# Kernel tuning notes

Measured on AMD Instinct MI355X. Metric: run time of the kernel, lower is better.

## Reference

```python
import jax, jax.numpy as jnp
import numpy as np

BN_EPS = 1e-5


def setup_inputs() -> dict:
    key = jax.random.key(0)
    ks = jax.random.split(key, 16)
    B, C, H, W = 8, 256, 56, 56
    Ci = C // 2  # inter_channels = 128
    s = lambda fan_in: 1.0 / np.sqrt(fan_in)
    return {
        "x": jax.random.normal(ks[0], (B, C, H, W), jnp.float32),
        # 1x1 convs stored as [out, in] matrices
        "g_w": jax.random.normal(ks[1], (Ci, C), jnp.float32) * s(C),
        "g_b": jax.random.normal(ks[2], (Ci,), jnp.float32) * s(C),
        "theta_w": jax.random.normal(ks[3], (Ci, C), jnp.float32) * s(C),
        "theta_b": jax.random.normal(ks[4], (Ci,), jnp.float32) * s(C),
        "phi_w": jax.random.normal(ks[5], (Ci, C), jnp.float32) * s(C),
        "phi_b": jax.random.normal(ks[6], (Ci,), jnp.float32) * s(C),
        # W_f: Conv2d(2*Ci -> 1, k=1)
        "wf_w": jax.random.normal(ks[7], (1, 2 * Ci), jnp.float32) * s(2 * Ci),
        "wf_b": jax.random.normal(ks[8], (1,), jnp.float32) * s(2 * Ci),
        # W_z conv (Ci -> C); source zero-inits; random here for a non-trivial baseline
        "wz_w": jax.random.normal(ks[9], (C, Ci), jnp.float32) * s(Ci),
        "wz_b": jax.random.normal(ks[10], (C,), jnp.float32) * s(Ci),
        # BatchNorm2d (eval mode) params/stats; source zero-inits gamma/beta, randomized here
        "bn_gamma": jax.random.normal(ks[11], (C,), jnp.float32) * 0.1 + 1.0,
        "bn_beta": jax.random.normal(ks[12], (C,), jnp.float32) * 0.1,
        "bn_mean": jax.random.normal(ks[13], (C,), jnp.float32) * 0.1,
        "bn_var": jax.random.uniform(ks[14], (C,), jnp.float32, 0.5, 1.5),
    }


def reference(x, g_w, g_b, theta_w, theta_b, phi_w, phi_b,
              wf_w, wf_b, wz_w, wz_b, bn_gamma, bn_beta, bn_mean, bn_var):
    B, C, H, W = x.shape
    N = H * W
    Ci = g_w.shape[0]
    xf = x.reshape(B, C, N)  # [B, C, N]

    # 1x1 convs over flattened spatial dim
    g_x = jnp.einsum('oc,bcn->bno', g_w, xf) + g_b            # [B, N, Ci]
    theta = jnp.einsum('oc,bcn->bon', theta_w, xf) + theta_b[:, None]  # [B, Ci, N]
    phi = jnp.einsum('oc,bcn->bon', phi_w, xf) + phi_b[:, None]        # [B, Ci, N]

    # W_f over the (repeat+concat) tensor decomposes exactly:
    # f[b,i,j] = relu( w_t . theta[b,:,i] + w_p . phi[b,:,j] + b_f )
    w_t, w_p = wf_w[0, :Ci], wf_w[0, Ci:]
    a = jnp.einsum('c,bcn->bn', w_t, theta)   # [B, N]
    bsc = jnp.einsum('c,bcn->bn', w_p, phi)   # [B, N]
    f = jax.nn.relu(a[:, :, None] + bsc[:, None, :] + wf_b[0])  # [B, N, N]

    y = jnp.matmul(f / N, g_x)                # [B, N, Ci]
    y = y.transpose(0, 2, 1)                  # [B, Ci, N]

    W_y = jnp.einsum('oc,bcn->bon', wz_w, y) + wz_b[:, None]   # [B, C, N]
    inv = bn_gamma / jnp.sqrt(bn_var + BN_EPS)
    W_y = (W_y - bn_mean[:, None]) * inv[:, None] + bn_beta[:, None]

    z = W_y + xf
    return z.reshape(B, C, H, W)
```

## Files before the change

kernel.cpp:

```cpp
#include <hip/hip_runtime.h>
#include <cfloat>
#include <math.h>

#define BATCH 8
#define CH 256
#define CI 128
#define NPIX 3136
#define NCHUNK 98
#define NB 4096
#define BN_EPS 1e-5f

typedef __attribute__((ext_vector_type(8))) short bf16x8;
typedef __attribute__((ext_vector_type(4))) float f32x4;

__device__ __forceinline__ float bf2f(unsigned short u) {
    union { unsigned int i; float f; } x; x.i = ((unsigned int)u) << 16; return x.f;
}
__device__ __forceinline__ unsigned short f2bf(float f) {
    union { float f; unsigned int i; } x; x.f = f;
    unsigned int u = x.i;
    return (unsigned short)((u + 0x7FFFu + ((u >> 16) & 1u)) >> 16);
}

__global__ __launch_bounds__(256) void k_fold(
    const float* __restrict__ wf_w,
    const float* __restrict__ theta_w, const float* __restrict__ theta_b,
    const float* __restrict__ phi_w,   const float* __restrict__ phi_b,
    const float* __restrict__ g_w,     const float* __restrict__ wz_w,
    float* __restrict__ ta_w, float* __restrict__ pb_w, float* __restrict__ biases,
    unsigned short* __restrict__ Bfrag_g, unsigned short* __restrict__ Bfrag_w)
{
    const int bk = blockIdx.x, tid = threadIdx.x;
    if (bk == 0) {
        float ta = 0.f, pb = 0.f;
        for (int c = 0; c < CI; ++c) {
            ta += wf_w[c]      * theta_w[c * CH + tid];
            pb += wf_w[CI + c] * phi_w[c * CH + tid];
        }
        ta_w[tid] = ta;
        pb_w[tid] = pb;
        if (tid == 0) {
            float tb = 0.f, pbb = 0.f;
            for (int c = 0; c < CI; ++c) {
                tb  += wf_w[c]      * theta_b[c];
                pbb += wf_w[CI + c] * phi_b[c];
            }
            biases[0] = tb;
            biases[1] = pbb;
        }
    } else if (bk <= 8) {
        const int base_pair = (bk - 1) * 8;
        for (int e = tid; e < 4096; e += 256) {
            int pp = e >> 9, lane = (e >> 3) & 63, j = e & 7;
            int pair = base_pair + pp;
            int ks = pair >> 3, nt = pair & 7;
            int k = ks * 32 + (lane >> 4) * 8 + j;
            int n = nt * 16 + (lane & 15);
            Bfrag_g[(size_t)pair * 512 + lane * 8 + j] = f2bf(g_w[n * CH + k]);
        }
    } else {
        const int base_pair = (bk - 9) * 8;
        for (int e = tid; e < 4096; e += 256) {
            int pp = e >> 9, lane = (e >> 3) & 63, j = e & 7;
            int pair = base_pair + pp;
            int ks = pair >> 4, nt = pair & 15;
            int k = ks * 32 + (lane >> 4) * 8 + j;
            int n = nt * 16 + (lane & 15);
            Bfrag_w[(size_t)pair * 512 + lane * 8 + j] = f2bf(wz_w[n * CI + k]);
        }
    }
}

__global__ __launch_bounds__(256) void k_gemm(
    const float* __restrict__ x,
    const unsigned short* __restrict__ Bfrag_g,
    const float* __restrict__ g_b,
    const float* __restrict__ ta_w, const float* __restrict__ pb_w,
    const float* __restrict__ biases,
    unsigned short* __restrict__ gxg,
    float* __restrict__ a_out, float* __restrict__ bsc_out)
{
    __shared__ float xs[CH][36];
    __shared__ unsigned short xsb[32 * 264];
    __shared__ float ra[8][32], rp[8][32];
    unsigned short* gout = (unsigned short*)&xs[0][0];

    const int b  = blockIdx.y;
    const int n0 = blockIdx.x * 32;
    const int tid = threadIdx.x;

    for (int t = tid; t < CH * 8; t += 256) {
        int c = t >> 3, n4 = t & 7;
        const float4* src = (const float4*)(x + ((size_t)b * CH + c) * NPIX + n0);
        *((float4*)&xs[c][n4 * 4]) = src[n4];
    }
    __syncthreads();

    const int p = tid & 31;
    const int g = tid >> 5;

    {
        float aa = 0.f, pp = 0.f;
#pragma unroll 8
        for (int cc = 0; cc < 32; ++cc) {
            int c = g * 32 + cc;
            float v = xs[c][p];
            aa += ta_w[c] * v;
            pp += pb_w[c] * v;
        }
        ra[g][p] = aa; rp[g][p] = pp;
    }
    {
        const int cbase = g * 32;
        unsigned int* dst = (unsigned int*)&xsb[p * 264 + cbase];
#pragma unroll
        for (int q = 0; q < 16; ++q) {
            float lo = xs[cbase + 2 * q][p];
            float hi = xs[cbase + 2 * q + 1][p];
            dst[q] = (unsigned int)f2bf(lo) | ((unsigned int)f2bf(hi) << 16);
        }
    }
    __syncthreads();

    if (tid < 32) {
        float sa = 0.f, sp = 0.f;
#pragma unroll
        for (int gg = 0; gg < 8; ++gg) { sa += ra[gg][tid]; sp += rp[gg][tid]; }
        a_out[b * NPIX + n0 + tid]   = sa + biases[0];
        bsc_out[b * NPIX + n0 + tid] = sp + biases[1];
    }

    const int w = tid >> 6, l = tid & 63, lm = l & 15, lq = l >> 4;
    f32x4 acc[2][2];
#pragma unroll
    for (int mi = 0; mi < 2; ++mi)
#pragma unroll
        for (int ni = 0; ni < 2; ++ni) acc[mi][ni] = (f32x4){0.f, 0.f, 0.f, 0.f};

#pragma unroll
    for (int ks = 0; ks < 8; ++ks) {
        bf16x8 a0 = *(const bf16x8*)&xsb[lm * 264 + ks * 32 + lq * 8];
        bf16x8 a1 = *(const bf16x8*)&xsb[(16 + lm) * 264 + ks * 32 + lq * 8];
        bf16x8 b0 = *(const bf16x8*)(Bfrag_g + ((size_t)(ks * 8 + w * 2) * 64 + l) * 8);
        bf16x8 b1 = *(const bf16x8*)(Bfrag_g + ((size_t)(ks * 8 + w * 2 + 1) * 64 + l) * 8);
        acc[0][0] = __builtin_amdgcn_mfma_f32_16x16x32_bf16(a0, b0, acc[0][0], 0, 0, 0);
        acc[0][1] = __builtin_amdgcn_mfma_f32_16x16x32_bf16(a0, b1, acc[0][1], 0, 0, 0);
        acc[1][0] = __builtin_amdgcn_mfma_f32_16x16x32_bf16(a1, b0, acc[1][0], 0, 0, 0);
        acc[1][1] = __builtin_amdgcn_mfma_f32_16x16x32_bf16(a1, b1, acc[1][1], 0, 0, 0);
    }
    __syncthreads();

#pragma unroll
    for (int mi = 0; mi < 2; ++mi)
#pragma unroll
        for (int ni = 0; ni < 2; ++ni) {
            int o = w * 32 + ni * 16 + lm;
            float gb = g_b[o];
#pragma unroll
            for (int r = 0; r < 4; ++r) {
                int m = mi * 16 + lq * 4 + r;
                gout[m * 136 + o] = f2bf(acc[mi][ni][r] + gb);
            }
        }
    __syncthreads();

    {
        const int n = tid >> 3, ch = tid & 7;
        const uint4* s = (const uint4*)&gout[n * 136 + ch * 16];
        uint4* d = (uint4*)(gxg + ((size_t)(b * NPIX + n0 + n)) * CI + ch * 16);
        d[0] = s[0]; d[1] = s[1];
    }
}

__global__ __launch_bounds__(1024) void k_bucketsort(
    const float* __restrict__ bsc,
    float* __restrict__ s_sorted, int* __restrict__ idx_sorted,
    int* __restrict__ bstart, float* __restrict__ params)
{
    __shared__ float vals[NPIX];
    __shared__ unsigned short qarr[NPIX];
    __shared__ int hist[NB];
    __shared__ int cnt[NB];
    __shared__ float red[1024];
    __shared__ float red2[1024];
    __shared__ float sh_min, sh_scale;

    const int b = blockIdx.x, tid = threadIdx.x;

    float lmin = FLT_MAX, lmax = -FLT_MAX;
    for (int i = tid; i < NPIX; i += 1024) {
        float v = bsc[b * NPIX + i];
        vals[i] = v;
        lmin = fminf(lmin, v);
        lmax = fmaxf(lmax, v);
    }
    red[tid] = lmin; red2[tid] = lmax;
    __syncthreads();
    for (int off = 512; off > 0; off >>= 1) {
        if (tid < off) {
            red[tid]  = fminf(red[tid],  red[tid + off]);
            red2[tid] = fmaxf(red2[tid], red2[tid + off]);
        }
        __syncthreads();
    }
    if (tid == 0) {
        float mn = red[0], mx = red2[0];
        float range = mx - mn;
        float scale = (range > 0.f) ? (float)NB / range : 0.f;
        sh_min = mn; sh_scale = scale;
        params[b * 2] = mn; params[b * 2 + 1] = scale;
    }
    for (int i = tid; i < NB; i += 1024) { hist[i] = 0; cnt[i] = 0; }
    __syncthreads();

    const float bmin = sh_min, scale = sh_scale;
    for (int i = tid; i < NPIX; i += 1024) {
        int q = (int)((vals[i] - bmin) * scale);
        q = (q < 0) ? 0 : ((q > NB - 1) ? NB - 1 : q);
        qarr[i] = (unsigned short)q;
        atomicAdd(&hist[q], 1);
    }
    __syncthreads();

    int* psum = (int*)red;
    const int base4 = tid * 4;
    int h0 = hist[base4], h1 = hist[base4 + 1], h2 = hist[base4 + 2], h3 = hist[base4 + 3];
    psum[tid] = h0 + h1 + h2 + h3;
    __syncthreads();
    for (int off = 1; off < 1024; off <<= 1) {
        int v = psum[tid];
        int w = (tid >= off) ? psum[tid - off] : 0;
        __syncthreads();
        psum[tid] = v + w;
        __syncthreads();
    }
    int excl = (tid == 0) ? 0 : psum[tid - 1];
    hist[base4]     = excl;
    hist[base4 + 1] = excl + h0;
    hist[base4 + 2] = excl + h0 + h1;
    hist[base4 + 3] = excl + h0 + h1 + h2;
    __syncthreads();

    for (int i = tid; i < NB; i += 1024) bstart[b * (NB + 1) + i] = hist[i];
    if (tid == 0) bstart[b * (NB + 1) + NB] = NPIX;

    for (int i = tid; i < NPIX; i += 1024) {
        int q = qarr[i];
        int pos = hist[q] + atomicAdd(&cnt[q], 1);
        s_sorted[b * NPIX + pos]   = vals[i];
        idx_sorted[b * NPIX + pos] = i;
    }
}

__global__ __launch_bounds__(128) void k_csum(
    const unsigned short* __restrict__ gxg,
    const float* __restrict__ s_sorted, const int* __restrict__ idx_sorted,
    float* __restrict__ CS1, float* __restrict__ CS2)
{
    __shared__ int   sidx[32];
    __shared__ float sval[32];
    const int b = blockIdx.y, c = blockIdx.x, o = threadIdx.x;
    const int base = b * NPIX + c * 32;
    if (o < 32) {
        sidx[o] = idx_sorted[base + o];
        sval[o] = s_sorted[base + o];
    }
    __syncthreads();

    float a1 = 0.f, a2 = 0.f;
#pragma unroll 8
    for (int rr = 0; rr < 32; ++rr) {
        float v = bf2f(gxg[((size_t)(b * NPIX + sidx[rr])) * CI + o]);
        a1 += v;
        a2 += sval[rr] * v;
    }
    CS1[(b * 100 + c) * CI + o] = a1;
    CS2[(b * 100 + c) * CI + o] = a2;
}

__global__ __launch_bounds__(128) void k_suffix(
    float* __restrict__ CS1, float* __restrict__ CS2)
{
    __shared__ float buf[NCHUNK * CI];
    const int b = blockIdx.x, tid = threadIdx.x;
    float* __restrict__ CS = blockIdx.y ? CS2 : CS1;

    for (int i = tid; i < NCHUNK * CI; i += 128) buf[i] = CS[b * 100 * CI + i];
    __syncthreads();
    {
        float acc = 0.f;
        for (int c = NCHUNK - 1; c >= 0; --c) {
            acc += buf[c * CI + tid];
            buf[c * CI + tid] = acc;
        }
    }
    __syncthreads();
    for (int i = tid; i < NCHUNK * CI; i += 128) CS[b * 100 * CI + i] = buf[i];
    CS[(b * 100 + 98) * CI + tid] = 0.f;
    CS[(b * 100 + 99) * CI + tid] = 0.f;
}

__global__ __launch_bounds__(256) void k_final(
    const float* __restrict__ x,
    const float* __restrict__ a_arr, const float* __restrict__ wf_b,
    const float* __restrict__ CS1, const float* __restrict__ CS2,
    const int* __restrict__ bstart, const float* __restrict__ params,
    const unsigned short* __restrict__ Bfrag_w,
    const float* __restrict__ wz_b,
    const float* __restrict__ bn_g, const float* __restrict__ bn_b,
    const float* __restrict__ bn_m, const float* __restrict__ bn_v,
    float* __restrict__ out)
{
    __shared__ unsigned short ys[32 * 136];
    __shared__ float Df[32 * 260];
    __shared__ int   rs[32];
    __shared__ float ts[32];

    const int b = blockIdx.y;
    const int n0 = blockIdx.x * 32;
    const int tid = threadIdx.x;

    if (tid < 32) {
        float t = a_arr[b * NPIX + n0 + tid] + wf_b[0];
        float bmin = params[b * 2], scale = params[b * 2 + 1];
        float fq = (-t - bmin) * scale;
        int kb = (int)(fq + 0.5f);
        kb = (kb < 0) ? 0 : ((kb > NB) ? NB : kb);
        int r = bstart[b * (NB + 1) + kb];
        int cstar = (r + 16) >> 5;
        cstar = (cstar > 98) ? 98 : cstar;
        rs[tid] = cstar;
        ts[tid] = t;
    }
    __syncthreads();

    const int o = tid & 127;
    const int h = tid >> 7;
    const float invN = 1.0f / (float)NPIX;

#pragma unroll 4
    for (int i = 0; i < 16; ++i) {
        int n = h * 16 + i;
        int cb = (b * 100 + rs[n]) * CI + o;
        float S1 = CS1[cb], S2 = CS2[cb];
        ys[n * 136 + o] = f2bf((ts[n] * S1 + S2) * invN);
    }
    __syncthreads();

    const int w = tid >> 6, l = tid & 63, lm = l & 15, lq = l >> 4;
    f32x4 acc[2][4];
#pragma unroll
    for (int mi = 0; mi < 2; ++mi)
#pragma unroll
        for (int ni = 0; ni < 4; ++ni) acc[mi][ni] = (f32x4){0.f, 0.f, 0.f, 0.f};

#pragma unroll
    for (int ks = 0; ks < 4; ++ks) {
        bf16x8 a0 = *(const bf16x8*)&ys[lm * 136 + ks * 32 + lq * 8];
        bf16x8 a1 = *(const bf16x8*)&ys[(16 + lm) * 136 + ks * 32 + lq * 8];
#pragma unroll
        for (int ni = 0; ni < 4; ++ni) {
            bf16x8 bb = *(const bf16x8*)(Bfrag_w + ((size_t)(ks * 16 + w * 4 + ni) * 64 + l) * 8);
            acc[0][ni] = __builtin_amdgcn_mfma_f32_16x16x32_bf16(a0, bb, acc[0][ni], 0, 0, 0);
            acc[1][ni] = __builtin_amdgcn_mfma_f32_16x16x32_bf16(a1, bb, acc[1][ni], 0, 0, 0);
        }
    }

#pragma unroll
    for (int mi = 0; mi < 2; ++mi)
#pragma unroll
        for (int ni = 0; ni < 4; ++ni) {
            int cc = w * 64 + ni * 16 + lm;
#pragma unroll
            for (int r = 0; r < 4; ++r) {
                int m = mi * 16 + lq * 4 + r;
                Df[m * 260 + cc] = acc[mi][ni][r];
            }
        }
    __syncthreads();

    const int cc = tid;
    const float inv  = bn_g[cc] * rsqrtf(bn_v[cc] + BN_EPS);
    const float bias = (wz_b[cc] - bn_m[cc]) * inv + bn_b[cc];

    const float4* xp = (const float4*)(x   + ((size_t)b * CH + cc) * NPIX + n0);
    float4*       op = (float4*)      (out + ((size_t)b * CH + cc) * NPIX + n0);
#pragma unroll
    for (int n4 = 0; n4 < 8; ++n4) {
        float4 xv = xp[n4];
        float4 ov;
        ov.x = Df[(n4 * 4 + 0) * 260 + cc] * inv + bias + xv.x;
        ov.y = Df[(n4 * 4 + 1) * 260 + cc] * inv + bias + xv.y;
        ov.z = Df[(n4 * 4 + 2) * 260 + cc] * inv + bias + xv.z;
        ov.w = Df[(n4 * 4 + 3) * 260 + cc] * inv + bias + xv.w;
        op[n4] = ov;
    }
}

extern "C" void kernel_launch(void* const* d_in, const int* in_sizes, int n_in,
                              void* d_out, int out_size, void* d_ws, size_t ws_size,
                              hipStream_t stream)
{
    const float* x       = (const float*)d_in[0];
    const float* g_w     = (const float*)d_in[1];
    const float* g_b     = (const float*)d_in[2];
    const float* theta_w = (const float*)d_in[3];
    const float* theta_b = (const float*)d_in[4];
    const float* phi_w   = (const float*)d_in[5];
    const float* phi_b   = (const float*)d_in[6];
    const float* wf_w    = (const float*)d_in[7];
    const float* wf_b    = (const float*)d_in[8];
    const float* wz_w    = (const float*)d_in[9];
    const float* wz_b    = (const float*)d_in[10];
    const float* bn_g    = (const float*)d_in[11];
    const float* bn_b    = (const float*)d_in[12];
    const float* bn_m    = (const float*)d_in[13];
    const float* bn_v    = (const float*)d_in[14];

    float* ws = (float*)d_ws;
    float* ta_w   = ws;
    float* pb_w   = ws + 256;
    float* biases = ws + 512;
    float* params = ws + 516;
    float* a_arr  = ws + 532;
    float* bsc      = a_arr + BATCH * NPIX;
    float* s_sorted = bsc + BATCH * NPIX;
    int*   idx_sorted = (int*)(s_sorted + BATCH * NPIX);
    int*   bstart   = idx_sorted + BATCH * NPIX;
    float* CS1    = (float*)(bstart + BATCH * (NB + 1));
    float* CS2    = CS1 + BATCH * 100 * CI;
    unsigned short* Bfrag_g = (unsigned short*)(CS2 + BATCH * 100 * CI);
    unsigned short* Bfrag_w = Bfrag_g + 32768;
    unsigned short* gxg = Bfrag_w + 32768;

    k_fold<<<17, 256, 0, stream>>>(wf_w, theta_w, theta_b, phi_w, phi_b,
                                   g_w, wz_w, ta_w, pb_w, biases,
                                   Bfrag_g, Bfrag_w);

    k_gemm<<<dim3(NCHUNK, BATCH), 256, 0, stream>>>(
        x, Bfrag_g, g_b, ta_w, pb_w, biases, gxg, a_arr, bsc);

    k_bucketsort<<<BATCH, 1024, 0, stream>>>(bsc, s_sorted, idx_sorted,
                                             bstart, params);

    k_csum<<<dim3(NCHUNK, BATCH), 128, 0, stream>>>(
        gxg, s_sorted, idx_sorted, CS1, CS2);

    k_suffix<<<dim3(BATCH, 2), 128, 0, stream>>>(CS1, CS2);

    k_final<<<dim3(NCHUNK, BATCH), 256, 0, stream>>>(
        x, a_arr, wf_b, CS1, CS2, bstart, params, Bfrag_w,
        wz_b, bn_g, bn_b, bn_m, bn_v, (float*)d_out);
}
```

Before: 160.9 us.

## Use wave-shuffle reductions and scans, parallelize suffix sum, fuse epilogues

```diff
diff --git a/kernel.cpp b/kernel.cpp
--- a/kernel.cpp
+++ b/kernel.cpp
@@ -100,25 +100,19 @@
     const int g = tid >> 5;
 
     {
+        const int cbase = g * 32;
         float aa = 0.f, pp = 0.f;
-#pragma unroll 8
-        for (int cc = 0; cc < 32; ++cc) {
-            int c = g * 32 + cc;
-            float v = xs[c][p];
-            aa += ta_w[c] * v;
-            pp += pb_w[c] * v;
+        unsigned int* dst = (unsigned int*)&xsb[p * 264 + cbase];
+#pragma unroll
+        for (int q = 0; q < 16; ++q) {
+            int c0 = cbase + 2 * q;
+            float lo = xs[c0][p];
+            float hi = xs[c0 + 1][p];
+            aa += ta_w[c0] * lo + ta_w[c0 + 1] * hi;
+            pp += pb_w[c0] * lo + pb_w[c0 + 1] * hi;
+            dst[q] = (unsigned int)f2bf(lo) | ((unsigned int)f2bf(hi) << 16);
         }
         ra[g][p] = aa; rp[g][p] = pp;
-    }
-    {
-        const int cbase = g * 32;
-        unsigned int* dst = (unsigned int*)&xsb[p * 264 + cbase];
-#pragma unroll
-        for (int q = 0; q < 16; ++q) {
-            float lo = xs[cbase + 2 * q][p];
-            float hi = xs[cbase + 2 * q + 1][p];
-            dst[q] = (unsigned int)f2bf(lo) | ((unsigned int)f2bf(hi) << 16);
-        }
     }
     __syncthreads();
 
@@ -148,7 +142,6 @@
         acc[1][0] = __builtin_amdgcn_mfma_f32_16x16x32_bf16(a1, b0, acc[1][0], 0, 0, 0);
         acc[1][1] = __builtin_amdgcn_mfma_f32_16x16x32_bf16(a1, b1, acc[1][1], 0, 0, 0);
     }
-    __syncthreads();
 
 #pragma unroll
     for (int mi = 0; mi < 2; ++mi)
@@ -177,78 +170,112 @@
     float* __restrict__ s_sorted, int* __restrict__ idx_sorted,
     int* __restrict__ bstart, float* __restrict__ params)
 {
-    __shared__ float vals[NPIX];
-    __shared__ unsigned short qarr[NPIX];
     __shared__ int hist[NB];
     __shared__ int cnt[NB];
-    __shared__ float red[1024];
-    __shared__ float red2[1024];
+    __shared__ float wmin[16], wmax[16];
+    __shared__ int wtot[16], woff[16];
     __shared__ float sh_min, sh_scale;
 
     const int b = blockIdx.x, tid = threadIdx.x;
-
+    const int lane = tid & 63, wid = tid >> 6;
+
+#pragma unroll
+    for (int k = 0; k < 4; ++k) { hist[tid + k * 1024] = 0; cnt[tid + k * 1024] = 0; }
+
+    float v[4];
     float lmin = FLT_MAX, lmax = -FLT_MAX;
-    for (int i = tid; i < NPIX; i += 1024) {
-        float v = bsc[b * NPIX + i];
-        vals[i] = v;
-        lmin = fminf(lmin, v);
-        lmax = fmaxf(lmax, v);
-    }
-    red[tid] = lmin; red2[tid] = lmax;
-    __syncthreads();
-    for (int off = 512; off > 0; off >>= 1) {
-        if (tid < off) {
-            red[tid]  = fminf(red[tid],  red[tid + off]);
-            red2[tid] = fmaxf(red2[tid], red2[tid + off]);
-        }
-        __syncthreads();
-    }
-    if (tid == 0) {
-        float mn = red[0], mx = red2[0];
-        float range = mx - mn;
-        float scale = (range > 0.f) ? (float)NB / range : 0.f;
-        sh_min = mn; sh_scale = scale;
-        params[b * 2] = mn; params[b * 2 + 1] = scale;
-    }
-    for (int i = tid; i < NB; i += 1024) { hist[i] = 0; cnt[i] = 0; }
+#pragma unroll
+    for (int k = 0; k < 4; ++k) {
+        int i = tid + k * 1024;
+        if (i < NPIX) {
+            float t = bsc[b * NPIX + i];
+            v[k] = t;
+            lmin = fminf(lmin, t);
+            lmax = fmaxf(lmax, t);
+        }
+    }
+#pragma unroll
+    for (int m = 32; m >= 1; m >>= 1) {
+        lmin = fminf(lmin, __shfl_xor(lmin, m));
+        lmax = fmaxf(lmax, __shfl_xor(lmax, m));
+    }
+    if (lane == 0) { wmin[wid] = lmin; wmax[wid] = lmax; }
+    __syncthreads();
+
+    if (tid < 16) {
+        float a = wmin[tid], c = wmax[tid];
+#pragma unroll
+        for (int m = 8; m >= 1; m >>= 1) {
+            a = fminf(a, __shfl_xor(a, m));
+            c = fmaxf(c, __shfl_xor(c, m));
+        }
+        if (tid == 0) {
+            float range = c - a;
+            float scale = (range > 0.f) ? (float)NB / range : 0.f;
+            sh_min = a; sh_scale = scale;
+            params[b * 2] = a; params[b * 2 + 1] = scale;
+        }
+    }
     __syncthreads();
 
     const float bmin = sh_min, scale = sh_scale;
-    for (int i = tid; i < NPIX; i += 1024) {
-        int q = (int)((vals[i] - bmin) * scale);
-        q = (q < 0) ? 0 : ((q > NB - 1) ? NB - 1 : q);
-        qarr[i] = (unsigned short)q;
-        atomicAdd(&hist[q], 1);
-    }
-    __syncthreads();
-
-    int* psum = (int*)red;
+    int q[4];
+#pragma unroll
+    for (int k = 0; k < 4; ++k) {
+        int i = tid + k * 1024;
+        if (i < NPIX) {
+            int qq = (int)((v[k] - bmin) * scale);
+            qq = (qq < 0) ? 0 : ((qq > NB - 1) ? NB - 1 : qq);
+            q[k] = qq;
+            atomicAdd(&hist[qq], 1);
+        }
+    }
+    __syncthreads();
+
     const int base4 = tid * 4;
     int h0 = hist[base4], h1 = hist[base4 + 1], h2 = hist[base4 + 2], h3 = hist[base4 + 3];
-    psum[tid] = h0 + h1 + h2 + h3;
-    __syncthreads();
-    for (int off = 1; off < 1024; off <<= 1) {
-        int v = psum[tid];
-        int w = (tid >= off) ? psum[tid - off] : 0;
-        __syncthreads();
-        psum[tid] = v + w;
-        __syncthreads();
-    }
-    int excl = (tid == 0) ? 0 : psum[tid - 1];
+    int s = h0 + h1 + h2 + h3;
+    int incl = s;
+#pragma unroll
+    for (int off = 1; off < 64; off <<= 1) {
+        int t = __shfl_up(incl, off);
+        if (lane >= off) incl += t;
+    }
+    if (lane == 63) wtot[wid] = incl;
+    __syncthreads();
+    if (tid < 16) {
+        int t = wtot[tid];
+        int wi = t;
+#pragma unroll
+        for (int off = 1; off < 16; off <<= 1) {
+            int u = __shfl_up(wi, off);
+            if (tid >= off) wi += u;
+        }
+        woff[tid] = wi - t;
+    }
+    __syncthreads();
+    int excl = woff[wid] + (incl - s);
     hist[base4]     = excl;
     hist[base4 + 1] = excl + h0;
     hist[base4 + 2] = excl + h0 + h1;
     hist[base4 + 3] = excl + h0 + h1 + h2;
     __syncthreads();
 
-    for (int i = tid; i < NB; i += 1024) bstart[b * (NB + 1) + i] = hist[i];
+#pragma unroll
+    for (int k = 0; k < 4; ++k) {
+        int i = tid + k * 1024;
+        bstart[b * (NB + 1) + i] = hist[i];
+    }
     if (tid == 0) bstart[b * (NB + 1) + NB] = NPIX;
 
-    for (int i = tid; i < NPIX; i += 1024) {
-        int q = qarr[i];
-        int pos = hist[q] + atomicAdd(&cnt[q], 1);
-        s_sorted[b * NPIX + pos]   = vals[i];
-        idx_sorted[b * NPIX + pos] = i;
+#pragma unroll
+    for (int k = 0; k < 4; ++k) {
+        int i = tid + k * 1024;
+        if (i < NPIX) {
+            int pos = hist[q[k]] + atomicAdd(&cnt[q[k]], 1);
+            s_sorted[b * NPIX + pos]   = v[k];
+            idx_sorted[b * NPIX + pos] = i;
+        }
     }
 }
 
@@ -278,26 +305,43 @@
     CS2[(b * 100 + c) * CI + o] = a2;
 }
 
-__global__ __launch_bounds__(128) void k_suffix(
+__global__ __launch_bounds__(1024) void k_suffix(
     float* __restrict__ CS1, float* __restrict__ CS2)
 {
     __shared__ float buf[NCHUNK * CI];
+    __shared__ float tot[8][CI];
     const int b = blockIdx.x, tid = threadIdx.x;
     float* __restrict__ CS = blockIdx.y ? CS2 : CS1;
 
-    for (int i = tid; i < NCHUNK * CI; i += 128) buf[i] = CS[b * 100 * CI + i];
-    __syncthreads();
+    for (int i = tid; i < NCHUNK * CI; i += 1024) buf[i] = CS[b * 100 * CI + i];
+    __syncthreads();
+
+    const int seg = tid >> 7, o = tid & 127;
+    const int c0 = seg * 13;
+    const int c1 = (seg == 7) ? NCHUNK : c0 + 13;
     {
         float acc = 0.f;
-        for (int c = NCHUNK - 1; c >= 0; --c) {
-            acc += buf[c * CI + tid];
-            buf[c * CI + tid] = acc;
-        }
-    }
-    __syncthreads();
-    for (int i = tid; i < NCHUNK * CI; i += 128) CS[b * 100 * CI + i] = buf[i];
-    CS[(b * 100 + 98) * CI + tid] = 0.f;
-    CS[(b * 100 + 99) * CI + tid] = 0.f;
+        for (int c = c1 - 1; c >= c0; --c) {
+            acc += buf[c * CI + o];
+            buf[c * CI + o] = acc;
+        }
+        tot[seg][o] = acc;
+    }
+    __syncthreads();
+    {
+        float off = 0.f;
+#pragma unroll
+        for (int s2 = 7; s2 >= 1; --s2) if (s2 > seg) off += tot[s2][o];
+        if (off != 0.f || seg < 7) {
+            for (int c = c0; c < c1; ++c) buf[c * CI + o] += off;
+        }
+    }
+    __syncthreads();
+    for (int i = tid; i < NCHUNK * CI; i += 1024) CS[b * 100 * CI + i] = buf[i];
+    if (tid < CI) {
+        CS[(b * 100 + 98) * CI + tid] = 0.f;
+        CS[(b * 100 + 99) * CI + tid] = 0.f;
+    }
 }
 
 __global__ __launch_bounds__(256) void k_final(
@@ -312,7 +356,6 @@
     float* __restrict__ out)
 {
     __shared__ unsigned short ys[32 * 136];
-    __shared__ float Df[32 * 260];
     __shared__ int   rs[32];
     __shared__ float ts[32];
 
@@ -348,6 +391,16 @@
     __syncthreads();
 
     const int w = tid >> 6, l = tid & 63, lm = l & 15, lq = l >> 4;
+
+    float invv[4], biasv[4];
+#pragma unroll
+    for (int ni = 0; ni < 4; ++ni) {
+        int cc = w * 64 + ni * 16 + lm;
+        float iv = bn_g[cc] * rsqrtf(bn_v[cc] + BN_EPS);
+        invv[ni] = iv;
+        biasv[ni] = (wz_b[cc] - bn_m[cc]) * iv + bn_b[cc];
+    }
+
     f32x4 acc[2][4];
 #pragma unroll
     for (int mi = 0; mi < 2; ++mi)
@@ -371,30 +424,16 @@
 #pragma unroll
         for (int ni = 0; ni < 4; ++ni) {
             int cc = w * 64 + ni * 16 + lm;
-#pragma unroll
-            for (int r = 0; r < 4; ++r) {
-                int m = mi * 16 + lq * 4 + r;
-                Df[m * 260 + cc] = acc[mi][ni][r];
-            }
-        }
-    __syncthreads();
-
-    const int cc = tid;
-    const float inv  = bn_g[cc] * rsqrtf(bn_v[cc] + BN_EPS);
-    const float bias = (wz_b[cc] - bn_m[cc]) * inv + bn_b[cc];
-
-    const float4* xp = (const float4*)(x   + ((size_t)b * CH + cc) * NPIX + n0);
-    float4*       op = (float4*)      (out + ((size_t)b * CH + cc) * NPIX + n0);
-#pragma unroll
-    for (int n4 = 0; n4 < 8; ++n4) {
-        float4 xv = xp[n4];
-        float4 ov;
-        ov.x = Df[(n4 * 4 + 0) * 260 + cc] * inv + bias + xv.x;
-        ov.y = Df[(n4 * 4 + 1) * 260 + cc] * inv + bias + xv.y;
-        ov.z = Df[(n4 * 4 + 2) * 260 + cc] * inv + bias + xv.z;
-        ov.w = Df[(n4 * 4 + 3) * 260 + cc] * inv + bias + xv.w;
-        op[n4] = ov;
-    }
+            int m  = mi * 16 + lq * 4;
+            size_t base = ((size_t)b * CH + cc) * NPIX + n0 + m;
+            const float4 xv = *(const float4*)(x + base);
+            float4 ov;
+            ov.x = acc[mi][ni][0] * invv[ni] + biasv[ni] + xv.x;
+            ov.y = acc[mi][ni][1] * invv[ni] + biasv[ni] + xv.y;
+            ov.z = acc[mi][ni][2] * invv[ni] + biasv[ni] + xv.z;
+            ov.w = acc[mi][ni][3] * invv[ni] + biasv[ni] + xv.w;
+            *(float4*)(out + base) = ov;
+        }
 }
 
 extern "C" void kernel_launch(void* const* d_in, const int* in_sizes, int n_in,
@@ -446,7 +485,7 @@
     k_csum<<<dim3(NCHUNK, BATCH), 128, 0, stream>>>(
         gxg, s_sorted, idx_sorted, CS1, CS2);
 
-    k_suffix<<<dim3(BATCH, 2), 128, 0, stream>>>(CS1, CS2);
+    k_suffix<<<dim3(BATCH, 2), 1024, 0, stream>>>(CS1, CS2);
 
     k_final<<<dim3(NCHUNK, BATCH), 256, 0, stream>>>(
         x, a_arr, wf_b, CS1, CS2, bstart, params, Bfrag_w,
```

Result: faster. 154.0 us (-4.3%).
